# Optimization experiments

Hardware: AMD Instinct MI355X
Metric: run time of the kernel (lower is better)

The kernel has to match this reference:

```python
import jax, jax.numpy as jnp
import numpy as np

N_NODES = 50000
EMBED = 128
HIDDEN = 256
N_EDGES = 800000
LN_EPS = 1e-5


def gcn_conv(x, src, dst, W, b, n_nodes):
    """PyG GCNConv with add_self_loops=True, normalize=True.
    x: [N, Fin]; src/dst: [E] int; W: [Fin, Fout]; b: [Fout]."""
    h = x @ W  # [N, Fout]
    loop = jnp.arange(n_nodes, dtype=src.dtype)
    src2 = jnp.concatenate([src, loop])  # [E+N]
    dst2 = jnp.concatenate([dst, loop])
    deg = jax.ops.segment_sum(jnp.ones_like(dst2, dtype=h.dtype), dst2, num_segments=n_nodes)
    dinv = jnp.where(deg > 0, jax.lax.rsqrt(jnp.where(deg > 0, deg, 1.0)), 0.0)
    norm = dinv[src2] * dinv[dst2]  # [E+N]
    msgs = h[src2] * norm[:, None]  # [E+N, Fout]
    out = jax.ops.segment_sum(msgs, dst2, num_segments=n_nodes)
    return out + b


def layer_norm(x, gamma, beta):
    mu = jnp.mean(x, axis=-1, keepdims=True)
    var = jnp.mean(jnp.square(x - mu), axis=-1, keepdims=True)
    return (x - mu) * jax.lax.rsqrt(var + LN_EPS) * gamma + beta


def setup_inputs() -> dict:
    key = jax.random.key(0)
    ks = jax.random.split(key, 12)
    x_ids = jax.random.randint(ks[0], (N_NODES, 1), 0, N_NODES)
    edge_index = jax.random.randint(ks[1], (2, N_EDGES), 0, N_NODES)
    embed_table = jax.random.normal(ks[2], (N_NODES, EMBED), dtype=jnp.float32)
    s1 = 1.0 / np.sqrt(EMBED)
    s2 = 1.0 / np.sqrt(HIDDEN)
    W1 = jax.random.uniform(ks[3], (EMBED, HIDDEN), jnp.float32, -s1, s1)
    b1 = jnp.zeros((HIDDEN,), jnp.float32)
    g1 = jnp.ones((HIDDEN,), jnp.float32)
    be1 = jnp.zeros((HIDDEN,), jnp.float32)
    W2 = jax.random.uniform(ks[4], (HIDDEN, EMBED), jnp.float32, -s2, s2)
    b2 = jnp.zeros((EMBED,), jnp.float32)
    g2 = jnp.ones((EMBED,), jnp.float32)
    be2 = jnp.zeros((EMBED,), jnp.float32)
    return {
        "x_ids": x_ids, "edge_index": edge_index,
        "embed_table": embed_table,
        "W1": W1, "b1": b1, "g1": g1, "be1": be1,
        "W2": W2, "b2": b2, "g2": g2, "be2": be2,
    }


def reference(x_ids, edge_index, embed_table, W1, b1, g1, be1, W2, b2, g2, be2):
    src, dst = edge_index[0], edge_index[1]
    x = embed_table[x_ids[:, 0]]  # [N, EMBED]
    x = gcn_conv(x, src, dst, W1, b1, N_NODES)  # [N, HIDDEN]
    x = layer_norm(jax.nn.relu(x), g1, be1)
    # dropout p=0.1 is identity in eval mode
    x = gcn_conv(x, src, dst, W2, b2, N_NODES)  # [N, EMBED]
    x = layer_norm(x, g2, be2)
    return x
```

## Files before the change

### kernel.cpp

```cpp
#include <hip/hip_runtime.h>
#include <hip/hip_bf16.h>
#include <cstdint>
#include <cstddef>

typedef short bf16x8 __attribute__((ext_vector_type(8)));
typedef float f32x4 __attribute__((ext_vector_type(4)));

#define BCAP 4096
#define NBK_MAX 512
#define CHUNK 8192
#define AGG_WAVES 8192

__device__ __forceinline__ void cvt2(unsigned int u, float& lo, float& hi) {
    union { unsigned int i; float f; } a, b;
    a.i = u << 16;
    b.i = u & 0xffff0000u;
    lo = a.f; hi = b.f;
}
__device__ __forceinline__ float bf2f(unsigned short s) {
    union { unsigned int i; float f; } c; c.i = ((unsigned int)s) << 16;
    return c.f;
}
__device__ __forceinline__ unsigned short f2bf(float f) {
    union { float f; unsigned int i; } c; c.f = f;
    unsigned int x = c.i;
    unsigned int r = (x + 0x7fffu + ((x >> 16) & 1u)) >> 16;
    return (unsigned short)r;
}

__global__ __launch_bounds__(256) void zero_k(int* __restrict__ flag,
                                              int* __restrict__ bucket_cnt, int nbk) {
    if (blockIdx.x == 0 && threadIdx.x == 0) flag[0] = 0;
    int i = blockIdx.x * 256 + threadIdx.x;
    if (i < nbk) bucket_cnt[i] = 0;
}

__global__ __launch_bounds__(256) void detect_k(const unsigned int* __restrict__ emb,
                                                int* __restrict__ flag) {
    __shared__ unsigned int red[256];
    int t = threadIdx.x;
    unsigned int m = 0;
    int base = blockIdx.x * 4096;
    #pragma unroll
    for (int i = 0; i < 16; ++i) {
        unsigned int u = emb[base + t + 256 * i];
        unsigned int lo = (u << 16) & 0x7fffffffu;
        m = m > lo ? m : lo;
    }
    red[t] = m; __syncthreads();
    for (int s = 128; s > 0; s >>= 1) {
        if (t < s) red[t] = red[t] > red[t + s] ? red[t] : red[t + s];
        __syncthreads();
    }
    if (t == 0 && red[0] > 0x4B000000u) atomicOr(flag, 1);
}

__device__ __forceinline__ unsigned short in_bf16(const void* p, size_t i, int f) {
    if (f) return f2bf(((const float*)p)[i]);
    return ((const unsigned short*)p)[i];
}
__device__ __forceinline__ float in_f32(const void* p, size_t i, int f) {
    if (f) return ((const float*)p)[i];
    return bf2f(((const unsigned short*)p)[i]);
}

__global__ __launch_bounds__(256) void pack_k(
    const void* __restrict__ W1, const void* __restrict__ W2,
    const void* b1, const void* g1, const void* be1,
    const void* b2, const void* g2, const void* be2,
    const int* __restrict__ flag,
    unsigned short* __restrict__ W1P, unsigned short* __restrict__ W2P,
    float* b1F, float* g1F, float* be1F, float* b2F, float* g2F, float* be2F) {
    int f = flag[0];
    if (blockIdx.x < 16) {
        int tid = blockIdx.x * 256 + threadIdx.x;
        int lane = tid & 63, kk = (tid >> 6) & 3, jt = tid >> 8;
        int col = jt * 16 + (lane & 15);
        int k0 = kk * 32 + (lane >> 4) * 8;
        unsigned short v[8];
        #pragma unroll
        for (int j = 0; j < 8; ++j) v[j] = in_bf16(W1, (size_t)(k0 + j) * 256 + col, f);
        #pragma unroll
        for (int j = 0; j < 8; ++j) W1P[(size_t)tid * 8 + j] = v[j];
    } else if (blockIdx.x < 32) {
        int tid = (blockIdx.x - 16) * 256 + threadIdx.x;
        int lane = tid & 63, kk = (tid >> 6) & 7, jt = tid >> 9;
        int col = jt * 16 + (lane & 15);
        int k0 = kk * 32 + (lane >> 4) * 8;
        unsigned short v[8];
        #pragma unroll
        for (int j = 0; j < 8; ++j) v[j] = in_bf16(W2, (size_t)(k0 + j) * 128 + col, f);
        #pragma unroll
        for (int j = 0; j < 8; ++j) W2P[(size_t)tid * 8 + j] = v[j];
    } else {
        int t = threadIdx.x;
        b1F[t]  = in_f32(b1, t, f);
        g1F[t]  = in_f32(g1, t, f);
        be1F[t] = in_f32(be1, t, f);
        if (t < 128) {
            b2F[t]  = in_f32(b2, t, f);
            g2F[t]  = in_f32(g2, t, f);
            be2F[t] = in_f32(be2, t, f);
        }
    }
}

__global__ __launch_bounds__(256) void bucket_scatter_k(
    const int* __restrict__ src, const int* __restrict__ dst,
    int* __restrict__ bucket_cnt, unsigned int* __restrict__ bucket, int E, int nbk) {
    __shared__ int hist[NBK_MAX];
    __shared__ int basel[NBK_MAX];
    int t = threadIdx.x;
    int e0 = blockIdx.x * CHUNK;
    int e1 = min(e0 + CHUNK, E);

    for (int i = t; i < nbk; i += 256) hist[i] = 0;
    __syncthreads();
    for (int e = e0 + t; e < e1; e += 256) {
        int d = __builtin_nontemporal_load(&dst[e]);
        atomicAdd(&hist[d >> 7], 1);
    }
    __syncthreads();
    for (int i = t; i < nbk; i += 256) {
        int c = hist[i];
        basel[i] = c ? atomicAdd(&bucket_cnt[i], c) : 0;
        hist[i] = 0;
    }
    __syncthreads();
    for (int e = e0 + t; e < e1; e += 256) {
        int d = __builtin_nontemporal_load(&dst[e]);
        int s = __builtin_nontemporal_load(&src[e]);
        int b = d >> 7;
        int slot = basel[b] + atomicAdd(&hist[b], 1);
        if (slot < BCAP)
            bucket[(size_t)b * BCAP + slot] = ((unsigned int)(d & 127) << 16) | (unsigned int)s;
    }
}

__global__ __launch_bounds__(256) void bscan_k(const int* __restrict__ bucket_cnt,
                                               int* __restrict__ boff, int nbk) {
    __shared__ int sh[256];
    __shared__ int carry;
    int t = threadIdx.x;
    if (t == 0) carry = 0;
    __syncthreads();
    for (int c0 = 0; c0 < nbk; c0 += 256) {
        int v = (c0 + t < nbk) ? min(bucket_cnt[c0 + t], BCAP) : 0;
        sh[t] = v; __syncthreads();
        for (int o = 1; o < 256; o <<= 1) {
            int u = (t >= o) ? sh[t - o] : 0;
            __syncthreads();
            sh[t] += u;
            __syncthreads();
        }
        if (c0 + t < nbk) boff[c0 + t] = carry + sh[t] - v;
        __syncthreads();
        if (t == 0) carry += sh[255];
        __syncthreads();
    }
}

__global__ __launch_bounds__(256) void bucket_fill_k(
    const unsigned int* __restrict__ bucket, const int* __restrict__ bucket_cnt,
    const int* __restrict__ boff,
    int* __restrict__ cnt, int* __restrict__ offs, float* __restrict__ dinv,
    unsigned short* __restrict__ csr, int N) {
    __shared__ int cnts[128], excl[128], curl[128];
    int t = threadIdx.x;
    int b = blockIdx.x;
    int base = b << 7;
    int nn = min(128, N - base);
    int total = min(bucket_cnt[b], BCAP);
    int boffb = boff[b];
    const unsigned int* bp = bucket + (size_t)b * BCAP;

    if (t < 128) cnts[t] = 0;
    __syncthreads();
    for (int i = t; i < total; i += 256)
        atomicAdd(&cnts[bp[i] >> 16], 1);
    __syncthreads();
    if (t < 128) excl[t] = cnts[t];
    __syncthreads();
    for (int o = 1; o < 128; o <<= 1) {
        int v = (t < 128 && t >= o) ? excl[t - o] : 0;
        __syncthreads();
        if (t < 128) excl[t] += v;
        __syncthreads();
    }
    if (t < nn) {
        int c = cnts[t];
        int ex = excl[t] - c;
        int node = base + t;
        cnt[node] = c;
        offs[node] = boffb + ex;
        dinv[node] = rsqrtf((float)(c + 1));
        curl[t] = ex;
    }
    __syncthreads();
    for (int i = t; i < total; i += 256) {
        unsigned int e = bp[i];
        int d = e >> 16;
        int slot = atomicAdd(&curl[d], 1);
        csr[boffb + slot] = (unsigned short)(e & 0xffffu);
    }
}

__global__ __launch_bounds__(256) void xs_k(
    const int* __restrict__ x_ids, const void* __restrict__ embed,
    const float* __restrict__ dinv, const int* __restrict__ flag,
    unsigned short* __restrict__ xs, int N)
{
    int tid = blockIdx.x * 256 + threadIdx.x;
    int n = tid >> 4;
    int c = tid & 15;
    if (n >= N) return;
    int id = x_ids[n];
    float dv = dinv[n];
    int f = flag[0];
    float v[8];
    if (f) {
        const float* er = (const float*)embed + (size_t)id * 128 + c * 8;
        float4 a = *(const float4*)er;
        float4 b = *(const float4*)(er + 4);
        v[0]=a.x; v[1]=a.y; v[2]=a.z; v[3]=a.w;
        v[4]=b.x; v[5]=b.y; v[6]=b.z; v[7]=b.w;
    } else {
        uint4 u = *(const uint4*)((const unsigned short*)embed + (size_t)id * 128 + c * 8);
        cvt2(u.x, v[0], v[1]); cvt2(u.y, v[2], v[3]);
        cvt2(u.z, v[4], v[5]); cvt2(u.w, v[6], v[7]);
    }
    union { unsigned short s[8]; uint4 u; } o;
    #pragma unroll
    for (int j = 0; j < 8; ++j) o.s[j] = f2bf(v[j] * dv);
    *(uint4*)&xs[(size_t)n * 128 + c * 8] = o.u;
}

__global__ __launch_bounds__(256) void agg1_k(
    const unsigned short* __restrict__ xs, const int* __restrict__ offs,
    const int* __restrict__ cnt, const unsigned short* __restrict__ csr,
    unsigned short* __restrict__ agg1s, int N)
{
    int lane = threadIdx.x & 63;
    int wid = blockIdx.x * 4 + (threadIdx.x >> 6);

    for (int n = wid; n < N; n += AGG_WAVES) {
        float ax[8], ay[8];
        #pragma unroll
        for (int i = 0; i < 8; ++i) { ax[i] = 0.f; ay[i] = 0.f; }
        {
            unsigned int r = *(const unsigned int*)&xs[(size_t)n * 128 + lane * 2];
            cvt2(r, ax[0], ay[0]);
        }
        int beg = offs[n];
        int end = beg + cnt[n];
        int j = beg;
        for (; j + 7 < end; j += 8) {
            unsigned int rr[8];
            #pragma unroll
            for (int i = 0; i < 8; ++i) {
                int s = csr[j + i];
                rr[i] = *(const unsigned int*)&xs[(size_t)s * 128 + lane * 2];
            }
            #pragma unroll
            for (int i = 0; i < 8; ++i) {
                float v0, v1; cvt2(rr[i], v0, v1);
                ax[i] += v0; ay[i] += v1;
            }
        }
        for (; j + 1 < end; j += 2) {
            int s0 = csr[j], s1 = csr[j + 1];
            unsigned int r0 = *(const unsigned int*)&xs[(size_t)s0 * 128 + lane * 2];
            unsigned int r1 = *(const unsigned int*)&xs[(size_t)s1 * 128 + lane * 2];
            float v0, v1; cvt2(r0, v0, v1); ax[0] += v0; ay[0] += v1;
            cvt2(r1, v0, v1); ax[1] += v0; ay[1] += v1;
        }
        if (j < end) {
            int s0 = csr[j];
            unsigned int r0 = *(const unsigned int*)&xs[(size_t)s0 * 128 + lane * 2];
            float v0, v1; cvt2(r0, v0, v1); ax[0] += v0; ay[0] += v1;
        }
        float o0 = ((ax[0]+ax[1])+(ax[2]+ax[3])) + ((ax[4]+ax[5])+(ax[6]+ax[7]));
        float o1 = ((ay[0]+ay[1])+(ay[2]+ay[3])) + ((ay[4]+ay[5])+(ay[6]+ay[7]));
        unsigned int pk = (unsigned int)f2bf(o0) | ((unsigned int)f2bf(o1) << 16);
        *(unsigned int*)&agg1s[(size_t)n * 128 + lane * 2] = pk;
    }
}

__global__ __launch_bounds__(256) void gemm_ln1_k(
    const unsigned short* __restrict__ agg1s, const unsigned short* __restrict__ W1P,
    const float* __restrict__ dinv, const float* __restrict__ b1,
    const float* __restrict__ g1, const float* __restrict__ be1,
    unsigned short* __restrict__ x1, int N)
{
    const int t = threadIdx.x;
    const int w = t >> 6;
    const int lane = t & 63;
    const int m = lane & 15;
    const int quad = lane >> 4;
    const int nb = blockIdx.x * 64;

    int node_a = nb + w * 16 + m;
    int idn = node_a < N ? node_a : N - 1;
    const unsigned short* er = agg1s + (size_t)idn * 128 + quad * 8;
    bf16x8 a[4];
    #pragma unroll
    for (int kk = 0; kk < 4; ++kk)
        a[kk] = *(const bf16x8*)(er + kk * 32);

    f32x4 acc[16];
    #pragma unroll
    for (int jt = 0; jt < 16; ++jt) acc[jt] = (f32x4){0.f, 0.f, 0.f, 0.f};

    #pragma unroll
    for (int kk = 0; kk < 4; ++kk) {
        #pragma unroll
        for (int jt = 0; jt < 16; ++jt) {
            bf16x8 b = *(const bf16x8*)(W1P + ((size_t)(jt * 4 + kk) * 64 + lane) * 8);
            acc[jt] = __builtin_amdgcn_mfma_f32_16x16x32_bf16(a[kk], b, acc[jt], 0, 0, 0);
        }
    }

    float bcol[16], gcol[16], ecol[16];
    #pragma unroll
    for (int jt = 0; jt < 16; ++jt) {
        bcol[jt] = b1[jt * 16 + m];
        gcol[jt] = g1[jt * 16 + m];
        ecol[jt] = be1[jt * 16 + m];
    }
    int base = nb + w * 16 + quad * 4;
    float4 dv4 = *(const float4*)&dinv[base < N ? base : 0];
    float dvr[4] = {dv4.x, dv4.y, dv4.z, dv4.w};

    #pragma unroll
    for (int reg = 0; reg < 4; ++reg) {
        int row = base + reg;
        float v[16];
        float s = 0.f, q = 0.f;
        #pragma unroll
        for (int jt = 0; jt < 16; ++jt) {
            float x = fmaxf(fmaf(acc[jt][reg], dvr[reg], bcol[jt]), 0.0f);
            v[jt] = x;
            s += x; q += x * x;
        }
        #pragma unroll
        for (int off = 1; off < 16; off <<= 1) {
            s += __shfl_xor(s, off);
            q += __shfl_xor(q, off);
        }
        float mu = s * (1.0f / 256.0f);
        float var = fmaxf(q * (1.0f / 256.0f) - mu * mu, 0.0f);
        float rstd = rsqrtf(var + 1e-5f);
        if (row < N) {
            unsigned short* xp = x1 + (size_t)row * 256 + m;
            #pragma unroll
            for (int jt = 0; jt < 16; ++jt)
                xp[jt * 16] = f2bf(fmaf((v[jt] - mu) * rstd, gcol[jt], ecol[jt]));
        }
    }
}

__global__ __launch_bounds__(256) void gemm2_k(
    const unsigned short* __restrict__ x1, const unsigned short* __restrict__ W2P,
    const float* __restrict__ dinv, unsigned short* __restrict__ h2s, int N)
{
    const int t = threadIdx.x;
    const int w = t >> 6;
    const int lane = t & 63;
    const int m = lane & 15;
    const int quad = lane >> 4;
    const int nb = blockIdx.x * 64;

    int node_a = nb + w * 16 + m;
    int idn = node_a < N ? node_a : N - 1;

    const unsigned short* er = x1 + (size_t)idn * 256 + quad * 8;
    bf16x8 a[8];
    #pragma unroll
    for (int kk = 0; kk < 8; ++kk)
        a[kk] = *(const bf16x8*)(er + kk * 32);

    f32x4 acc[8];
    #pragma unroll
    for (int jt = 0; jt < 8; ++jt) acc[jt] = (f32x4){0.f, 0.f, 0.f, 0.f};

    #pragma unroll
    for (int kk = 0; kk < 8; ++kk) {
        #pragma unroll
        for (int jt = 0; jt < 8; ++jt) {
            bf16x8 b = *(const bf16x8*)(W2P + ((size_t)(jt * 8 + kk) * 64 + lane) * 8);
            acc[jt] = __builtin_amdgcn_mfma_f32_16x16x32_bf16(a[kk], b, acc[jt], 0, 0, 0);
        }
    }

    int base = nb + w * 16 + quad * 4;
    float4 dv4 = *(const float4*)&dinv[base < N ? base : 0];
    float dvr[4] = {dv4.x, dv4.y, dv4.z, dv4.w};
    #pragma unroll
    for (int reg = 0; reg < 4; ++reg) {
        int node_r = base + reg;
        if (node_r < N) {
            unsigned short* hp = h2s + (size_t)node_r * 128 + m;
            #pragma unroll
            for (int jt = 0; jt < 8; ++jt)
                hp[jt * 16] = f2bf(acc[jt][reg] * dvr[reg]);
        }
    }
}

__global__ __launch_bounds__(256) void agg_ln2_k(
    const unsigned short* __restrict__ h2s, const int* __restrict__ offs,
    const int* __restrict__ cnt, const unsigned short* __restrict__ csr,
    const float* __restrict__ dinv, const float* __restrict__ b2,
    const float* __restrict__ g2, const float* __restrict__ be2,
    const int* __restrict__ flag, void* __restrict__ out, int N)
{
    int lane = threadIdx.x & 63;
    int wid = blockIdx.x * 4 + (threadIdx.x >> 6);
    int f = flag[0];

    for (int n = wid; n < N; n += AGG_WAVES) {
        float ax[8], ay[8];
        #pragma unroll
        for (int i = 0; i < 8; ++i) { ax[i] = 0.f; ay[i] = 0.f; }
        {
            unsigned int r = *(const unsigned int*)&h2s[(size_t)n * 128 + lane * 2];
            cvt2(r, ax[0], ay[0]);
        }
        int beg = offs[n];
        int end = beg + cnt[n];
        int j = beg;
        for (; j + 7 < end; j += 8) {
            unsigned int rr[8];
            #pragma unroll
            for (int i = 0; i < 8; ++i) {
                int s = csr[j + i];
                rr[i] = *(const unsigned int*)&h2s[(size_t)s * 128 + lane * 2];
            }
            #pragma unroll
            for (int i = 0; i < 8; ++i) {
                float v0, v1; cvt2(rr[i], v0, v1);
                ax[i] += v0; ay[i] += v1;
            }
        }
        for (; j + 1 < end; j += 2) {
            int s0 = csr[j], s1 = csr[j + 1];
            unsigned int r0 = *(const unsigned int*)&h2s[(size_t)s0 * 128 + lane * 2];
            unsigned int r1 = *(const unsigned int*)&h2s[(size_t)s1 * 128 + lane * 2];
            float v0, v1; cvt2(r0, v0, v1); ax[0] += v0; ay[0] += v1;
            cvt2(r1, v0, v1); ax[1] += v0; ay[1] += v1;
        }
        if (j < end) {
            int s0 = csr[j];
            unsigned int r0 = *(const unsigned int*)&h2s[(size_t)s0 * 128 + lane * 2];
            float v0, v1; cvt2(r0, v0, v1); ax[0] += v0; ay[0] += v1;
        }
        float sum0 = ((ax[0]+ax[1])+(ax[2]+ax[3])) + ((ax[4]+ax[5])+(ax[6]+ax[7]));
        float sum1 = ((ay[0]+ay[1])+(ay[2]+ay[3])) + ((ay[4]+ay[5])+(ay[6]+ay[7]));
        float dv = dinv[n];
        float2 bv = *(const float2*)&b2[lane * 2];
        float x0 = fmaf(sum0, dv, bv.x);
        float x1 = fmaf(sum1, dv, bv.y);
        float s = x0 + x1;
        float q = x0*x0 + x1*x1;
        #pragma unroll
        for (int off = 32; off > 0; off >>= 1) {
            s += __shfl_xor(s, off);
            q += __shfl_xor(q, off);
        }
        float mu = s * (1.0f / 128.0f);
        float var = fmaxf(q * (1.0f / 128.0f) - mu * mu, 0.0f);
        float rstd = rsqrtf(var + 1e-5f);
        float2 gv = *(const float2*)&g2[lane * 2];
        float2 ev = *(const float2*)&be2[lane * 2];
        float o0 = fmaf((x0 - mu) * rstd, gv.x, ev.x);
        float o1 = fmaf((x1 - mu) * rstd, gv.y, ev.y);
        if (f) {
            *(float2*)&((float*)out)[(size_t)n * 128 + lane * 2] = make_float2(o0, o1);
        } else {
            unsigned int packed = (unsigned int)f2bf(o0) | ((unsigned int)f2bf(o1) << 16);
            *(unsigned int*)&((unsigned short*)out)[(size_t)n * 128 + lane * 2] = packed;
        }
    }
}

extern "C" void kernel_launch(void* const* d_in, const int* in_sizes, int n_in,
                              void* d_out, int out_size, void* d_ws, size_t ws_size,
                              hipStream_t stream) {
    const int N = in_sizes[0];
    const int E = in_sizes[1] / 2;
    const int nbk = (N + 127) >> 7;

    const int* x_ids = (const int*)d_in[0];
    const int* src = (const int*)d_in[1];
    const int* dst = src + E;
    const void* embed = d_in[2];
    const void* W1 = d_in[3];
    const void* b1 = d_in[4];
    const void* g1 = d_in[5];
    const void* be1 = d_in[6];
    const void* W2 = d_in[7];
    const void* b2 = d_in[8];
    const void* g2 = d_in[9];
    const void* be2 = d_in[10];

    char* w = (char*)d_ws;
    auto take = [&](size_t bytes) { char* p = w; w += (bytes + 255) & ~(size_t)255; return p; };
    int* flag             = (int*)take(4);
    unsigned short* W1P   = (unsigned short*)take(65536);
    unsigned short* W2P   = (unsigned short*)take(65536);
    float* b1F  = (float*)take(1024);
    float* g1F  = (float*)take(1024);
    float* be1F = (float*)take(1024);
    float* b2F  = (float*)take(512);
    float* g2F  = (float*)take(512);
    float* be2F = (float*)take(512);
    int* bucket_cnt = (int*)take((size_t)nbk * 4);
    int* boff       = (int*)take((size_t)nbk * 4);
    unsigned int* bucket = (unsigned int*)take((size_t)nbk * BCAP * 4);
    int* cnt    = (int*)take((size_t)N * 4);
    int* offs   = (int*)take((size_t)N * 4);
    unsigned short* csr = (unsigned short*)take((size_t)E * 2);
    float* dinv = (float*)take(((size_t)N + 64) * 4);
    unsigned short* xs    = (unsigned short*)take((size_t)N * 128 * 2);
    unsigned short* agg1s = (unsigned short*)take((size_t)N * 128 * 2);
    unsigned short* x1    = (unsigned short*)take((size_t)N * 256 * 2);
    unsigned short* h2s   = agg1s;

    zero_k  <<<(nbk + 255) / 256, 256, 0, stream>>>(flag, bucket_cnt, nbk);
    detect_k<<<16, 256, 0, stream>>>((const unsigned int*)embed, flag);
    pack_k  <<<33, 256, 0, stream>>>(W1, W2, b1, g1, be1, b2, g2, be2, flag,
                                     W1P, W2P, b1F, g1F, be1F, b2F, g2F, be2F);

    bucket_scatter_k<<<(E + CHUNK - 1) / CHUNK, 256, 0, stream>>>(src, dst, bucket_cnt, bucket, E, nbk);
    bscan_k         <<<1, 256, 0, stream>>>(bucket_cnt, boff, nbk);
    bucket_fill_k   <<<nbk, 256, 0, stream>>>(bucket, bucket_cnt, boff, cnt, offs, dinv, csr, N);

    xs_k      <<<(N * 16 + 255) / 256, 256, 0, stream>>>(x_ids, embed, dinv, flag, xs, N);
    agg1_k    <<<AGG_WAVES / 4, 256, 0, stream>>>(xs, offs, cnt, csr, agg1s, N);
    gemm_ln1_k<<<(N + 63) / 64, 256, 0, stream>>>(agg1s, W1P, dinv, b1F, g1F, be1F, x1, N);

    gemm2_k   <<<(N + 63) / 64, 256, 0, stream>>>(x1, W2P, dinv, h2s, N);
    agg_ln2_k <<<AGG_WAVES / 4, 256, 0, stream>>>(h2s, offs, cnt, csr, dinv, b2F, g2F, be2F, flag, d_out, N);
}
```

Measured before the change: 258.3 us.

## Fuse layer-1 aggregation into GEMM+LN, merge xs into bucket fill, drop scan

Aggregates layer-1 neighbor sums directly into a shared-memory tile inside the GEMM+LayerNorm kernel, so the agg1s intermediate no longer goes through global memory. It also folds the embedding gather and scaling into bucket_fill_k, and merges bucket zeroing into detect_k. The bucket prefix scan is replaced by fixed per-bucket CSR offsets (b*BCAP), which sizes the CSR to nbk*BCAP. This removes several launches and one full intermediate round trip through memory. The cost is that each aggregation wave now handles 16 nodes serially inside a GEMM block, which may hide gather latency less well than the old grid-strided aggregation kernel. Flag detection now samples only the first 4096 words of the embedding.

```diff
diff --git a/kernel.cpp b/kernel.cpp
--- a/kernel.cpp
+++ b/kernel.cpp
@@ -28,22 +28,16 @@
     return (unsigned short)r;
 }
 
-__global__ __launch_bounds__(256) void zero_k(int* __restrict__ flag,
-                                              int* __restrict__ bucket_cnt, int nbk) {
-    if (blockIdx.x == 0 && threadIdx.x == 0) flag[0] = 0;
-    int i = blockIdx.x * 256 + threadIdx.x;
-    if (i < nbk) bucket_cnt[i] = 0;
-}
-
 __global__ __launch_bounds__(256) void detect_k(const unsigned int* __restrict__ emb,
-                                                int* __restrict__ flag) {
+                                                int* __restrict__ flag,
+                                                int* __restrict__ bucket_cnt, int nbk) {
     __shared__ unsigned int red[256];
     int t = threadIdx.x;
+    for (int i = t; i < nbk; i += 256) bucket_cnt[i] = 0;
     unsigned int m = 0;
-    int base = blockIdx.x * 4096;
     #pragma unroll
     for (int i = 0; i < 16; ++i) {
-        unsigned int u = emb[base + t + 256 * i];
+        unsigned int u = emb[t + 256 * i];
         unsigned int lo = (u << 16) & 0x7fffffffu;
         m = m > lo ? m : lo;
     }
@@ -52,7 +46,7 @@
         if (t < s) red[t] = red[t] > red[t + s] ? red[t] : red[t + s];
         __syncthreads();
     }
-    if (t == 0 && red[0] > 0x4B000000u) atomicOr(flag, 1);
+    if (t == 0) flag[0] = (red[0] > 0x4B000000u) ? 1 : 0;
 }
 
 __device__ __forceinline__ unsigned short in_bf16(const void* p, size_t i, int f) {
@@ -137,41 +131,20 @@
     }
 }
 
-__global__ __launch_bounds__(256) void bscan_k(const int* __restrict__ bucket_cnt,
-                                               int* __restrict__ boff, int nbk) {
-    __shared__ int sh[256];
-    __shared__ int carry;
-    int t = threadIdx.x;
-    if (t == 0) carry = 0;
-    __syncthreads();
-    for (int c0 = 0; c0 < nbk; c0 += 256) {
-        int v = (c0 + t < nbk) ? min(bucket_cnt[c0 + t], BCAP) : 0;
-        sh[t] = v; __syncthreads();
-        for (int o = 1; o < 256; o <<= 1) {
-            int u = (t >= o) ? sh[t - o] : 0;
-            __syncthreads();
-            sh[t] += u;
-            __syncthreads();
-        }
-        if (c0 + t < nbk) boff[c0 + t] = carry + sh[t] - v;
-        __syncthreads();
-        if (t == 0) carry += sh[255];
-        __syncthreads();
-    }
-}
-
 __global__ __launch_bounds__(256) void bucket_fill_k(
     const unsigned int* __restrict__ bucket, const int* __restrict__ bucket_cnt,
-    const int* __restrict__ boff,
     int* __restrict__ cnt, int* __restrict__ offs, float* __restrict__ dinv,
-    unsigned short* __restrict__ csr, int N) {
+    unsigned short* __restrict__ csr,
+    const int* __restrict__ x_ids, const void* __restrict__ embed,
+    const int* __restrict__ flag, unsigned short* __restrict__ xs, int N) {
     __shared__ int cnts[128], excl[128], curl[128];
+    __shared__ float dinvl[128];
     int t = threadIdx.x;
     int b = blockIdx.x;
     int base = b << 7;
     int nn = min(128, N - base);
     int total = min(bucket_cnt[b], BCAP);
-    int boffb = boff[b];
+    int cbase = b * BCAP;
     const unsigned int* bp = bucket + (size_t)b * BCAP;
 
     if (t < 128) cnts[t] = 0;
@@ -192,8 +165,10 @@
         int ex = excl[t] - c;
         int node = base + t;
         cnt[node] = c;
-        offs[node] = boffb + ex;
-        dinv[node] = rsqrtf((float)(c + 1));
+        offs[node] = cbase + ex;
+        float dv = rsqrtf((float)(c + 1));
+        dinv[node] = dv;
+        dinvl[t] = dv;
         curl[t] = ex;
     }
     __syncthreads();
@@ -201,97 +176,42 @@
         unsigned int e = bp[i];
         int d = e >> 16;
         int slot = atomicAdd(&curl[d], 1);
-        csr[boffb + slot] = (unsigned short)(e & 0xffffu);
-    }
-}
-
-__global__ __launch_bounds__(256) void xs_k(
-    const int* __restrict__ x_ids, const void* __restrict__ embed,
-    const float* __restrict__ dinv, const int* __restrict__ flag,
-    unsigned short* __restrict__ xs, int N)
-{
-    int tid = blockIdx.x * 256 + threadIdx.x;
-    int n = tid >> 4;
-    int c = tid & 15;
-    if (n >= N) return;
-    int id = x_ids[n];
-    float dv = dinv[n];
+        csr[cbase + slot] = (unsigned short)(e & 0xffffu);
+    }
     int f = flag[0];
-    float v[8];
-    if (f) {
-        const float* er = (const float*)embed + (size_t)id * 128 + c * 8;
-        float4 a = *(const float4*)er;
-        float4 b = *(const float4*)(er + 4);
-        v[0]=a.x; v[1]=a.y; v[2]=a.z; v[3]=a.w;
-        v[4]=b.x; v[5]=b.y; v[6]=b.z; v[7]=b.w;
-    } else {
-        uint4 u = *(const uint4*)((const unsigned short*)embed + (size_t)id * 128 + c * 8);
-        cvt2(u.x, v[0], v[1]); cvt2(u.y, v[2], v[3]);
-        cvt2(u.z, v[4], v[5]); cvt2(u.w, v[6], v[7]);
-    }
-    union { unsigned short s[8]; uint4 u; } o;
-    #pragma unroll
-    for (int j = 0; j < 8; ++j) o.s[j] = f2bf(v[j] * dv);
-    *(uint4*)&xs[(size_t)n * 128 + c * 8] = o.u;
-}
-
-__global__ __launch_bounds__(256) void agg1_k(
+    for (int i = t; i < nn * 16; i += 256) {
+        int nl = i >> 4, c = i & 15;
+        int n = base + nl;
+        int id = x_ids[n];
+        float dv = dinvl[nl];
+        float v[8];
+        if (f) {
+            const float* er = (const float*)embed + (size_t)id * 128 + c * 8;
+            float4 a = *(const float4*)er;
+            float4 bb = *(const float4*)(er + 4);
+            v[0]=a.x; v[1]=a.y; v[2]=a.z; v[3]=a.w;
+            v[4]=bb.x; v[5]=bb.y; v[6]=bb.z; v[7]=bb.w;
+        } else {
+            uint4 u = *(const uint4*)((const unsigned short*)embed + (size_t)id * 128 + c * 8);
+            cvt2(u.x, v[0], v[1]); cvt2(u.y, v[2], v[3]);
+            cvt2(u.z, v[4], v[5]); cvt2(u.w, v[6], v[7]);
+        }
+        union { unsigned short s[8]; uint4 u; } o;
+        #pragma unroll
+        for (int j = 0; j < 8; ++j) o.s[j] = f2bf(v[j] * dv);
+        *(uint4*)&xs[(size_t)n * 128 + c * 8] = o.u;
+    }
+}
+
+#define ROWP 136
+__global__ __launch_bounds__(256) void agg_gemm_ln1_k(
     const unsigned short* __restrict__ xs, const int* __restrict__ offs,
     const int* __restrict__ cnt, const unsigned short* __restrict__ csr,
-    unsigned short* __restrict__ agg1s, int N)
+    const unsigned short* __restrict__ W1P, const float* __restrict__ dinv,
+    const float* __restrict__ b1, const float* __restrict__ g1,
+    const float* __restrict__ be1, unsigned short* __restrict__ x1, int N)
 {
-    int lane = threadIdx.x & 63;
-    int wid = blockIdx.x * 4 + (threadIdx.x >> 6);
-
-    for (int n = wid; n < N; n += AGG_WAVES) {
-        float ax[8], ay[8];
-        #pragma unroll
-        for (int i = 0; i < 8; ++i) { ax[i] = 0.f; ay[i] = 0.f; }
-        {
-            unsigned int r = *(const unsigned int*)&xs[(size_t)n * 128 + lane * 2];
-            cvt2(r, ax[0], ay[0]);
-        }
-        int beg = offs[n];
-        int end = beg + cnt[n];
-        int j = beg;
-        for (; j + 7 < end; j += 8) {
-            unsigned int rr[8];
-            #pragma unroll
-            for (int i = 0; i < 8; ++i) {
-                int s = csr[j + i];
-                rr[i] = *(const unsigned int*)&xs[(size_t)s * 128 + lane * 2];
-            }
-            #pragma unroll
-            for (int i = 0; i < 8; ++i) {
-                float v0, v1; cvt2(rr[i], v0, v1);
-                ax[i] += v0; ay[i] += v1;
-            }
-        }
-        for (; j + 1 < end; j += 2) {
-            int s0 = csr[j], s1 = csr[j + 1];
-            unsigned int r0 = *(const unsigned int*)&xs[(size_t)s0 * 128 + lane * 2];
-            unsigned int r1 = *(const unsigned int*)&xs[(size_t)s1 * 128 + lane * 2];
-            float v0, v1; cvt2(r0, v0, v1); ax[0] += v0; ay[0] += v1;
-            cvt2(r1, v0, v1); ax[1] += v0; ay[1] += v1;
-        }
-        if (j < end) {
-            int s0 = csr[j];
-            unsigned int r0 = *(const unsigned int*)&xs[(size_t)s0 * 128 + lane * 2];
-            float v0, v1; cvt2(r0, v0, v1); ax[0] += v0; ay[0] += v1;
-        }
-        float o0 = ((ax[0]+ax[1])+(ax[2]+ax[3])) + ((ax[4]+ax[5])+(ax[6]+ax[7]));
-        float o1 = ((ay[0]+ay[1])+(ay[2]+ay[3])) + ((ay[4]+ay[5])+(ay[6]+ay[7]));
-        unsigned int pk = (unsigned int)f2bf(o0) | ((unsigned int)f2bf(o1) << 16);
-        *(unsigned int*)&agg1s[(size_t)n * 128 + lane * 2] = pk;
-    }
-}
-
-__global__ __launch_bounds__(256) void gemm_ln1_k(
-    const unsigned short* __restrict__ agg1s, const unsigned short* __restrict__ W1P,
-    const float* __restrict__ dinv, const float* __restrict__ b1,
-    const float* __restrict__ g1, const float* __restrict__ be1,
-    unsigned short* __restrict__ x1, int N)
-{
+    __shared__ unsigned short aggl[64 * ROWP];
     const int t = threadIdx.x;
     const int w = t >> 6;
     const int lane = t & 63;
@@ -299,13 +219,56 @@
     const int quad = lane >> 4;
     const int nb = blockIdx.x * 64;
 
-    int node_a = nb + w * 16 + m;
-    int idn = node_a < N ? node_a : N - 1;
-    const unsigned short* er = agg1s + (size_t)idn * 128 + quad * 8;
+    for (int i = 0; i < 16; ++i) {
+        int n = nb + w * 16 + i;
+        float o0 = 0.f, o1 = 0.f;
+        if (n < N) {
+            float ax[8], ay[8];
+            #pragma unroll
+            for (int k = 0; k < 8; ++k) { ax[k] = 0.f; ay[k] = 0.f; }
+            {
+                unsigned int r = *(const unsigned int*)&xs[(size_t)n * 128 + lane * 2];
+                cvt2(r, ax[0], ay[0]);
+            }
+            int beg = offs[n];
+            int end = beg + cnt[n];
+            int j = beg;
+            for (; j + 7 < end; j += 8) {
+                unsigned int rr[8];
+                #pragma unroll
+                for (int k = 0; k < 8; ++k) {
+                    int s = csr[j + k];
+                    rr[k] = *(const unsigned int*)&xs[(size_t)s * 128 + lane * 2];
+                }
+                #pragma unroll
+                for (int k = 0; k < 8; ++k) {
+                    float v0, v1; cvt2(rr[k], v0, v1);
+                    ax[k] += v0; ay[k] += v1;
+                }
+            }
+            for (; j + 1 < end; j += 2) {
+                int s0 = csr[j], s1 = csr[j + 1];
+                unsigned int r0 = *(const unsigned int*)&xs[(size_t)s0 * 128 + lane * 2];
+                unsigned int r1 = *(const unsigned int*)&xs[(size_t)s1 * 128 + lane * 2];
+                float v0, v1; cvt2(r0, v0, v1); ax[0] += v0; ay[0] += v1;
+                cvt2(r1, v0, v1); ax[1] += v0; ay[1] += v1;
+            }
+            if (j < end) {
+                int s0 = csr[j];
+                unsigned int r0 = *(const unsigned int*)&xs[(size_t)s0 * 128 + lane * 2];
+                float v0, v1; cvt2(r0, v0, v1); ax[0] += v0; ay[0] += v1;
+            }
+            o0 = ((ax[0]+ax[1])+(ax[2]+ax[3])) + ((ax[4]+ax[5])+(ax[6]+ax[7]));
+            o1 = ((ay[0]+ay[1])+(ay[2]+ay[3])) + ((ay[4]+ay[5])+(ay[6]+ay[7]));
+        }
+        unsigned int pk = (unsigned int)f2bf(o0) | ((unsigned int)f2bf(o1) << 16);
+        *(unsigned int*)&aggl[(w * 16 + i) * ROWP + lane * 2] = pk;
+    }
+
     bf16x8 a[4];
     #pragma unroll
     for (int kk = 0; kk < 4; ++kk)
-        a[kk] = *(const bf16x8*)(er + kk * 32);
+        a[kk] = *(const bf16x8*)&aggl[(w * 16 + m) * ROWP + quad * 8 + kk * 32];
 
     f32x4 acc[16];
     #pragma unroll
@@ -515,29 +478,25 @@
     float* g2F  = (float*)take(512);
     float* be2F = (float*)take(512);
     int* bucket_cnt = (int*)take((size_t)nbk * 4);
-    int* boff       = (int*)take((size_t)nbk * 4);
     unsigned int* bucket = (unsigned int*)take((size_t)nbk * BCAP * 4);
     int* cnt    = (int*)take((size_t)N * 4);
     int* offs   = (int*)take((size_t)N * 4);
-    unsigned short* csr = (unsigned short*)take((size_t)E * 2);
+    unsigned short* csr = (unsigned short*)take((size_t)nbk * BCAP * 2);
     float* dinv = (float*)take(((size_t)N + 64) * 4);
-    unsigned short* xs    = (unsigned short*)take((size_t)N * 128 * 2);
-    unsigned short* agg1s = (unsigned short*)take((size_t)N * 128 * 2);
-    unsigned short* x1    = (unsigned short*)take((size_t)N * 256 * 2);
-    unsigned short* h2s   = agg1s;
-
-    zero_k  <<<(nbk + 255) / 256, 256, 0, stream>>>(flag, bucket_cnt, nbk);
-    detect_k<<<16, 256, 0, stream>>>((const unsigned int*)embed, flag);
+    unsigned short* xs  = (unsigned short*)take((size_t)N * 128 * 2);
+    unsigned short* x1  = (unsigned short*)take((size_t)N * 256 * 2);
+    unsigned short* h2s = xs;
+
+    detect_k<<<1, 256, 0, stream>>>((const unsigned int*)embed, flag, bucket_cnt, nbk);
     pack_k  <<<33, 256, 0, stream>>>(W1, W2, b1, g1, be1, b2, g2, be2, flag,
                                      W1P, W2P, b1F, g1F, be1F, b2F, g2F, be2F);
 
     bucket_scatter_k<<<(E + CHUNK - 1) / CHUNK, 256, 0, stream>>>(src, dst, bucket_cnt, bucket, E, nbk);
-    bscan_k         <<<1, 256, 0, stream>>>(bucket_cnt, boff, nbk);
-    bucket_fill_k   <<<nbk, 256, 0, stream>>>(bucket, bucket_cnt, boff, cnt, offs, dinv, csr, N);
-
-    xs_k      <<<(N * 16 + 255) / 256, 256, 0, stream>>>(x_ids, embed, dinv, flag, xs, N);
-    agg1_k    <<<AGG_WAVES / 4, 256, 0, stream>>>(xs, offs, cnt, csr, agg1s, N);
-    gemm_ln1_k<<<(N + 63) / 64, 256, 0, stream>>>(agg1s, W1P, dinv, b1F, g1F, be1F, x1, N);
+    bucket_fill_k   <<<nbk, 256, 0, stream>>>(bucket, bucket_cnt, cnt, offs, dinv, csr,
+                                              x_ids, embed, flag, xs, N);
+
+    agg_gemm_ln1_k<<<(N + 63) / 64, 256, 0, stream>>>(xs, offs, cnt, csr, W1P, dinv,
+                                                      b1F, g1F, be1F, x1, N);
 
     gemm2_k   <<<(N + 63) / 64, 256, 0, stream>>>(x1, W2P, dinv, h2s, N);
     agg_ln2_k <<<AGG_WAVES / 4, 256, 0, stream>>>(h2s, offs, cnt, csr, dinv, b2F, g2F, be2F, flag, d_out, N);
```

After: 306.6 us. 1.19x slower.
